# Optimization experiments

Hardware: AMD Instinct MI355X
Metric: run time of the kernel (lower is better)

The kernel has to match this reference:

```python
import jax, jax.numpy as jnp
import numpy as np

ALPHA = 0.2  # LeakyReLU negative slope
NEG_INF = jnp.float32(-9e15)


def setup_inputs() -> dict:
    key = jax.random.key(0)
    k1, k2, k3, k4, k5, k6 = jax.random.split(key, 6)
    B, N, F_in, F_out = 8, 2048, 256, 64
    h = jax.random.normal(k1, (B, N, F_in), dtype=jnp.float32)
    adj = jax.random.randint(k2, (B, N, N), 0, 2, dtype=jnp.int32)
    level = jax.random.uniform(k3, (B, N), dtype=jnp.float32)
    node_type = jax.random.uniform(k4, (B, N, N), dtype=jnp.float32)
    W = jax.random.normal(k5, (F_in, F_out), dtype=jnp.float32) * 1.414 / np.sqrt(F_in)
    a = jax.random.normal(k6, (2 * F_out, 1), dtype=jnp.float32) * 1.414 / np.sqrt(2 * F_out)
    return {"h": h, "adj": adj, "level": level, "node_type": node_type, "W": W, "a": a}


def reference(h, adj, level, node_type, W, a):
    # h: [B,N,Fin], adj/node_type: [B,N,N], level: [B,N], W: [Fin,Fout], a: [2*Fout,1]
    F_out = W.shape[1]
    Wh = jnp.einsum('bnf,fo->bno', h, W)  # [B,N,Fout]
    # Additive attention decomposed: e[b,i,j] = a1.Wh_i + a2.Wh_j (no O(N^2*2F) tensor)
    a1 = a[:F_out, 0]
    a2 = a[F_out:, 0]
    f1 = Wh @ a1  # [B,N]
    f2 = Wh @ a2  # [B,N]
    e = jax.nn.leaky_relu(f1[:, :, None] + f2[:, None, :], negative_slope=ALPHA)  # [B,N,N]
    # gat_our=True path: node_type scales scores, level scales Wh
    e = e * node_type
    Wh = Wh * level[:, :, None]
    attention = jnp.where(adj > 0, e, NEG_INF)
    attention = jax.nn.softmax(attention, axis=1)  # faithful: original softmax over dim=1
    # dropout p=0 / eval mode -> identity
    h_prime = jnp.einsum('bij,bjo->bio', attention, Wh)  # [B,N,Fout]
    return jax.nn.relu(h_prime)  # concat=True
```

## Files before the change

kernel.cpp:

```cpp
#include <hip/hip_runtime.h>

#define BB 8
#define NN 2048
#define FIN 256
#define FO 64

typedef short short8_t __attribute__((ext_vector_type(8)));
typedef float float4_t __attribute__((ext_vector_type(4)));

__device__ __forceinline__ unsigned short f2bf(float x) {
  unsigned int u = __float_as_uint(x);
  unsigned int r = (u + 0x7fffu + ((u >> 16) & 1u)) >> 16;
  return (unsigned short)r;
}

__global__ __launch_bounds__(256) void k1_gemm(
    const float* __restrict__ h,
    const float* __restrict__ level,
    const float* __restrict__ W,
    const float* __restrict__ a,
    float* __restrict__ V, float* __restrict__ f1, float* __restrict__ f2)
{
  __shared__ float hs[64 * 65];
  __shared__ float wsm[64 * 64];
  __shared__ float parts[2 * 1040];
  int t = threadIdx.x;
  int b = blockIdx.x >> 5;
  int i0 = (blockIdx.x & 31) * 64;
  int ti = t & 15, to = t >> 4;
  int srow = t >> 2;
  int sf0 = (t & 3) * 16;
  float acc[4][4] = {};

  for (int fc = 0; fc < FIN; fc += 64) {
    const float* hp = h + (size_t)(b * NN + i0 + srow) * FIN + fc + sf0;
    float4 h0 = *(const float4*)hp;
    float4 h1 = *(const float4*)(hp + 4);
    float4 h2 = *(const float4*)(hp + 8);
    float4 h3 = *(const float4*)(hp + 12);
    float* hd = &hs[srow * 65 + sf0];
    hd[0] = h0.x; hd[1] = h0.y; hd[2] = h0.z; hd[3] = h0.w;
    hd[4] = h1.x; hd[5] = h1.y; hd[6] = h1.z; hd[7] = h1.w;
    hd[8] = h2.x; hd[9] = h2.y; hd[10] = h2.z; hd[11] = h2.w;
    hd[12] = h3.x; hd[13] = h3.y; hd[14] = h3.z; hd[15] = h3.w;

    const float* wp = W + (size_t)(fc + srow) * FO + sf0;
    float4 w0 = *(const float4*)wp;
    float4 w1 = *(const float4*)(wp + 4);
    float4 w2 = *(const float4*)(wp + 8);
    float4 w3 = *(const float4*)(wp + 12);
    float* wd = &wsm[srow * 64 + sf0];
    *(float4*)(wd + 0) = w0; *(float4*)(wd + 4) = w1;
    *(float4*)(wd + 8) = w2; *(float4*)(wd + 12) = w3;
    __syncthreads();

    #pragma unroll 4
    for (int f = 0; f < 64; ++f) {
      float hv0 = hs[(ti * 4 + 0) * 65 + f];
      float hv1 = hs[(ti * 4 + 1) * 65 + f];
      float hv2 = hs[(ti * 4 + 2) * 65 + f];
      float hv3 = hs[(ti * 4 + 3) * 65 + f];
      float4 wv = *(const float4*)&wsm[f * 64 + to * 4];
      acc[0][0] += hv0 * wv.x; acc[0][1] += hv0 * wv.y; acc[0][2] += hv0 * wv.z; acc[0][3] += hv0 * wv.w;
      acc[1][0] += hv1 * wv.x; acc[1][1] += hv1 * wv.y; acc[1][2] += hv1 * wv.z; acc[1][3] += hv1 * wv.w;
      acc[2][0] += hv2 * wv.x; acc[2][1] += hv2 * wv.y; acc[2][2] += hv2 * wv.z; acc[2][3] += hv2 * wv.w;
      acc[3][0] += hv3 * wv.x; acc[3][1] += hv3 * wv.y; acc[3][2] += hv3 * wv.z; acc[3][3] += hv3 * wv.w;
    }
    __syncthreads();
  }

  float a1f0 = a[to * 4 + 0], a1f1 = a[to * 4 + 1];
  float a1f2 = a[to * 4 + 2], a1f3 = a[to * 4 + 3];
  float a2f0 = a[64 + to * 4 + 0], a2f1 = a[64 + to * 4 + 1];
  float a2f2 = a[64 + to * 4 + 2], a2f3 = a[64 + to * 4 + 3];
  #pragma unroll
  for (int r = 0; r < 4; ++r) {
    float p1 = acc[r][0] * a1f0 + acc[r][1] * a1f1 + acc[r][2] * a1f2 + acc[r][3] * a1f3;
    float p2 = acc[r][0] * a2f0 + acc[r][1] * a2f1 + acc[r][2] * a2f2 + acc[r][3] * a2f3;
    parts[to * 65 + ti * 4 + r] = p1;
    parts[1040 + to * 65 + ti * 4 + r] = p2;
  }
  __syncthreads();
  if (t < 64) {
    float s1 = 0.f, s2 = 0.f;
    #pragma unroll
    for (int g = 0; g < 16; ++g) { s1 += parts[g * 65 + t]; s2 += parts[1040 + g * 65 + t]; }
    f1[b * NN + i0 + t] = s1;
    f2[b * NN + i0 + t] = s2;
  }

  #pragma unroll
  for (int r = 0; r < 4; ++r) {
    float lv = level[b * NN + i0 + ti * 4 + r];
    float4 vv;
    vv.x = acc[r][0] * lv; vv.y = acc[r][1] * lv; vv.z = acc[r][2] * lv; vv.w = acc[r][3] * lv;
    *(float4*)&V[(size_t)(b * NN + i0 + ti * 4 + r) * FO + to * 4] = vv;
  }
}

template <int STORE_U>
__global__ __launch_bounds__(512) void k2_stats(
    const int* __restrict__ adj,
    const float* __restrict__ ntp,
    const float* __restrict__ f1,
    const float* __restrict__ f2,
    const float* __restrict__ V,
    unsigned short* __restrict__ vf,
    unsigned short* __restrict__ u_bf,
    unsigned char* __restrict__ bits)
{
  __shared__ float red[512 * 9];
  __shared__ float sinv[64];
  int t = threadIdx.x;
  int b = blockIdx.x >> 5;
  int jt = blockIdx.x & 31;
  int j0 = jt * 64;
  int tj = t & 7, isub = t >> 3;
  int j8 = j0 + tj * 8;

  float f2v[8];
  #pragma unroll
  for (int e = 0; e < 8; ++e) f2v[e] = f2[b * NN + j8 + e];
  float acc8[8] = {0, 0, 0, 0, 0, 0, 0, 0};

  for (int i = isub; i < NN; i += 64) {
    size_t base = (size_t)(b * NN + i);
    const int* ap = adj + base * NN + j8;
    int4 a0 = *(const int4*)ap;
    int4 a1 = *(const int4*)(ap + 4);
    const float* npp = ntp + base * NN + j8;
    float4 n0 = *(const float4*)npp;
    float4 n1 = *(const float4*)(npp + 4);
    float f1v = f1[base];
    float ntf[8] = {n0.x, n0.y, n0.z, n0.w, n1.x, n1.y, n1.z, n1.w};
    int am[8] = {a0.x, a0.y, a0.z, a0.w, a1.x, a1.y, a1.z, a1.w};
    float uv[8];
    unsigned int mb = 0;
    #pragma unroll
    for (int e = 0; e < 8; ++e) {
      float x = f1v + f2v[e];
      x = fmaxf(x, 0.2f * x);
      float E = x * ntf[e];
      bool m = am[e] > 0;
      float u = m ? __expf(E) : 0.0f;
      uv[e] = u;
      acc8[e] += u;
      mb |= (m ? 1u : 0u) << e;
    }
    if (STORE_U) {
      uint4 pk;
      pk.x = (unsigned int)f2bf(uv[0]) | ((unsigned int)f2bf(uv[1]) << 16);
      pk.y = (unsigned int)f2bf(uv[2]) | ((unsigned int)f2bf(uv[3]) << 16);
      pk.z = (unsigned int)f2bf(uv[4]) | ((unsigned int)f2bf(uv[5]) << 16);
      pk.w = (unsigned int)f2bf(uv[6]) | ((unsigned int)f2bf(uv[7]) << 16);
      *(uint4*)(u_bf + base * NN + j8) = pk;
    } else {
      bits[base * (NN / 8) + jt * 8 + tj] = (unsigned char)mb;
    }
  }

  #pragma unroll
  for (int e = 0; e < 8; ++e) red[t * 9 + e] = acc8[e];
  __syncthreads();
  if (t < 64) {
    int tjj = t >> 3, ee = t & 7;
    float s = 0.f;
    for (int is = 0; is < 64; ++is) s += red[(is * 8 + tjj) * 9 + ee];
    sinv[t] = (s > 0.f) ? (1.0f / s) : 0.0f;
  }
  __syncthreads();

  int kl = t >> 8;
  int ng = (t >> 6) & 3;
  int l = t & 63;
  int kk = jt * 2 + kl;
  int jb = kl * 32 + ((l >> 4) * 8);
  int o = ng * 16 + (l & 15);
  unsigned int pk[4];
  #pragma unroll
  for (int p = 0; p < 4; ++p) {
    int jr0 = jb + 2 * p, jr1 = jb + 2 * p + 1;
    float v0 = V[(size_t)(b * NN + j0 + jr0) * FO + o] * sinv[jr0];
    float v1 = V[(size_t)(b * NN + j0 + jr1) * FO + o] * sinv[jr1];
    pk[p] = (unsigned int)f2bf(v0) | ((unsigned int)f2bf(v1) << 16);
  }
  *(uint4*)(vf + (size_t)(((b * 64 + kk) * 4 + ng) * 64 + l) * 8) =
      make_uint4(pk[0], pk[1], pk[2], pk[3]);
}

__global__ __launch_bounds__(256) void k3_agg_u(
    const unsigned short* __restrict__ u_bf,
    const unsigned short* __restrict__ vf,
    float* __restrict__ outp)
{
  __shared__ float red[4 * 16 * 68];
  int t = threadIdx.x;
  int b = blockIdx.x >> 7;
  int i0 = (blockIdx.x & 127) * 16;
  int w = t >> 6, l = t & 63;
  int col = l & 15, quad = l >> 4;
  const unsigned short* urow = u_bf + (size_t)(b * NN + i0 + col) * NN + quad * 8;
  const unsigned short* vbase = vf + (size_t)(b * 64) * 2048 + l * 8;
  float4_t acc0 = {0, 0, 0, 0}, acc1 = {0, 0, 0, 0}, acc2 = {0, 0, 0, 0}, acc3 = {0, 0, 0, 0};

  for (int s = 0; s < 16; ++s) {
    int kk = w * 16 + s;
    short8_t A = *(const short8_t*)(urow + kk * 32);
    const unsigned short* vb = vbase + (size_t)kk * 2048;
    short8_t bf0 = *(const short8_t*)(vb);
    short8_t bf1 = *(const short8_t*)(vb + 512);
    short8_t bf2 = *(const short8_t*)(vb + 1024);
    short8_t bf3 = *(const short8_t*)(vb + 1536);
    acc0 = __builtin_amdgcn_mfma_f32_16x16x32_bf16(A, bf0, acc0, 0, 0, 0);
    acc1 = __builtin_amdgcn_mfma_f32_16x16x32_bf16(A, bf1, acc1, 0, 0, 0);
    acc2 = __builtin_amdgcn_mfma_f32_16x16x32_bf16(A, bf2, acc2, 0, 0, 0);
    acc3 = __builtin_amdgcn_mfma_f32_16x16x32_bf16(A, bf3, acc3, 0, 0, 0);
  }

  #pragma unroll
  for (int r = 0; r < 4; ++r) {
    int rowi = quad * 4 + r;
    red[w * 1088 + rowi * 68 + 0 + col] = acc0[r];
    red[w * 1088 + rowi * 68 + 16 + col] = acc1[r];
    red[w * 1088 + rowi * 68 + 32 + col] = acc2[r];
    red[w * 1088 + rowi * 68 + 48 + col] = acc3[r];
  }
  __syncthreads();

  int row = t >> 4, o4 = (t & 15) * 4;
  const float* rp = &red[row * 68 + o4];
  float4 s0 = *(const float4*)(rp);
  float4 s1 = *(const float4*)(rp + 1088);
  float4 s2 = *(const float4*)(rp + 2176);
  float4 s3 = *(const float4*)(rp + 3264);
  float4 o;
  o.x = fmaxf(s0.x + s1.x + s2.x + s3.x, 0.0f);
  o.y = fmaxf(s0.y + s1.y + s2.y + s3.y, 0.0f);
  o.z = fmaxf(s0.z + s1.z + s2.z + s3.z, 0.0f);
  o.w = fmaxf(s0.w + s1.w + s2.w + s3.w, 0.0f);
  *(float4*)&outp[(size_t)(b * NN + i0 + row) * FO + o4] = o;
}

__global__ __launch_bounds__(256) void k3_agg_b(
    const float* __restrict__ ntp,
    const unsigned char* __restrict__ bits,
    const float* __restrict__ f1,
    const float* __restrict__ f2,
    const unsigned short* __restrict__ vf,
    float* __restrict__ outp)
{
  __shared__ float red[4 * 16 * 68];
  int t = threadIdx.x;
  int b = blockIdx.x >> 7;
  int i0 = (blockIdx.x & 127) * 16;
  int w = t >> 6, l = t & 63;
  int col = l & 15, quad = l >> 4;
  int gi = b * NN + i0 + col;
  float f1v = f1[gi];
  const float* ntrow = ntp + (size_t)gi * NN;
  const unsigned char* brow = bits + (size_t)gi * (NN / 8);
  float4_t acc0 = {0, 0, 0, 0}, acc1 = {0, 0, 0, 0}, acc2 = {0, 0, 0, 0}, acc3 = {0, 0, 0, 0};

  for (int s = 0; s < 16; ++s) {
    int kk = w * 16 + s;
    int jq = kk * 32 + quad * 8;
    unsigned int m8 = brow[jq >> 3];
    float4 n0 = *(const float4*)(ntrow + jq);
    float4 n1 = *(const float4*)(ntrow + jq + 4);
    float4 g0 = *(const float4*)(f2 + b * NN + jq);
    float4 g1 = *(const float4*)(f2 + b * NN + jq + 4);
    float f2v[8] = {g0.x, g0.y, g0.z, g0.w, g1.x, g1.y, g1.z, g1.w};
    float ntf[8] = {n0.x, n0.y, n0.z, n0.w, n1.x, n1.y, n1.z, n1.w};
    union { unsigned int u[4]; short8_t v; } A;
    #pragma unroll
    for (int p = 0; p < 4; ++p) {
      int e0 = 2 * p, e1 = 2 * p + 1;
      float x0 = f1v + f2v[e0]; x0 = fmaxf(x0, 0.2f * x0);
      float u0 = ((m8 >> e0) & 1u) ? __expf(x0 * ntf[e0]) : 0.0f;
      float x1 = f1v + f2v[e1]; x1 = fmaxf(x1, 0.2f * x1);
      float u1 = ((m8 >> e1) & 1u) ? __expf(x1 * ntf[e1]) : 0.0f;
      A.u[p] = (unsigned int)f2bf(u0) | ((unsigned int)f2bf(u1) << 16);
    }
    const unsigned short* vb = vf + (size_t)(b * 64 + kk) * 2048 + l * 8;
    short8_t bf0 = *(const short8_t*)(vb);
    short8_t bf1 = *(const short8_t*)(vb + 512);
    short8_t bf2 = *(const short8_t*)(vb + 1024);
    short8_t bf3 = *(const short8_t*)(vb + 1536);
    acc0 = __builtin_amdgcn_mfma_f32_16x16x32_bf16(A.v, bf0, acc0, 0, 0, 0);
    acc1 = __builtin_amdgcn_mfma_f32_16x16x32_bf16(A.v, bf1, acc1, 0, 0, 0);
    acc2 = __builtin_amdgcn_mfma_f32_16x16x32_bf16(A.v, bf2, acc2, 0, 0, 0);
    acc3 = __builtin_amdgcn_mfma_f32_16x16x32_bf16(A.v, bf3, acc3, 0, 0, 0);
  }

  #pragma unroll
  for (int r = 0; r < 4; ++r) {
    int rowi = quad * 4 + r;
    red[w * 1088 + rowi * 68 + 0 + col] = acc0[r];
    red[w * 1088 + rowi * 68 + 16 + col] = acc1[r];
    red[w * 1088 + rowi * 68 + 32 + col] = acc2[r];
    red[w * 1088 + rowi * 68 + 48 + col] = acc3[r];
  }
  __syncthreads();

  int row = t >> 4, o4 = (t & 15) * 4;
  const float* rp = &red[row * 68 + o4];
  float4 s0 = *(const float4*)(rp);
  float4 s1 = *(const float4*)(rp + 1088);
  float4 s2 = *(const float4*)(rp + 2176);
  float4 s3 = *(const float4*)(rp + 3264);
  float4 o;
  o.x = fmaxf(s0.x + s1.x + s2.x + s3.x, 0.0f);
  o.y = fmaxf(s0.y + s1.y + s2.y + s3.y, 0.0f);
  o.z = fmaxf(s0.z + s1.z + s2.z + s3.z, 0.0f);
  o.w = fmaxf(s0.w + s1.w + s2.w + s3.w, 0.0f);
  *(float4*)&outp[(size_t)(b * NN + i0 + row) * FO + o4] = o;
}

extern "C" void kernel_launch(void* const* d_in, const int* in_sizes, int n_in,
                              void* d_out, int out_size, void* d_ws, size_t ws_size,
                              hipStream_t stream) {
  const float* h = (const float*)d_in[0];
  const int* adj = (const int*)d_in[1];
  const float* level = (const float*)d_in[2];
  const float* ntm = (const float*)d_in[3];
  const float* W = (const float*)d_in[4];
  const float* a = (const float*)d_in[5];
  float* outp = (float*)d_out;

  float* V = (float*)d_ws;
  float* f1 = V + (size_t)BB * NN * FO;
  float* f2 = f1 + BB * NN;
  unsigned short* vf = (unsigned short*)(f2 + BB * NN);
  char* tail = (char*)(vf + (size_t)BB * NN * FO);
  size_t fixed = (size_t)(tail - (char*)d_ws);
  size_t need_u = fixed + (size_t)BB * NN * NN * 2;
  bool big = (ws_size >= need_u);

  k1_gemm<<<256, 256, 0, stream>>>(h, level, W, a, V, f1, f2);
  if (big) {
    unsigned short* u_bf = (unsigned short*)tail;
    k2_stats<1><<<256, 512, 0, stream>>>(adj, ntm, f1, f2, V, vf, u_bf, nullptr);
    k3_agg_u<<<1024, 256, 0, stream>>>(u_bf, vf, outp);
  } else {
    unsigned char* bits = (unsigned char*)tail;
    k2_stats<0><<<256, 512, 0, stream>>>(adj, ntm, f1, f2, V, vf, nullptr, bits);
    k3_agg_b<<<1024, 256, 0, stream>>>(ntm, bits, f1, f2, vf, outp);
  }
}
```

Baseline: 351.7 us.

## Split column-stats pass over row chunks with atomics and separate V packing

The stats kernel now splits the 2048 rows into 8 chunks, giving 2048 blocks instead of 256, and accumulates column sums into a zeroed global buffer with atomicAdd. The V normalization and bf16 packing move into a new kernel that runs after all partial sums are complete. The projection GEMM is also retiled to 16 rows per block, reading W directly from global memory, which gives 1024 blocks. The aim is to fill the GPU's compute units on the bandwidth-heavy adjacency and node_type scan, at the cost of two extra launches and atomic traffic.

```diff
diff --git a/kernel.cpp b/kernel.cpp
--- a/kernel.cpp
+++ b/kernel.cpp
@@ -12,6 +12,10 @@
   unsigned int u = __float_as_uint(x);
   unsigned int r = (u + 0x7fffu + ((u >> 16) & 1u)) >> 16;
   return (unsigned short)r;
+}
+
+__global__ __launch_bounds__(256) void k0_zero(float* __restrict__ scol) {
+  scol[blockIdx.x * 256 + threadIdx.x] = 0.0f;
 }
 
 __global__ __launch_bounds__(256) void k1_gemm(
@@ -21,99 +25,77 @@
     const float* __restrict__ a,
     float* __restrict__ V, float* __restrict__ f1, float* __restrict__ f2)
 {
-  __shared__ float hs[64 * 65];
-  __shared__ float wsm[64 * 64];
-  __shared__ float parts[2 * 1040];
-  int t = threadIdx.x;
-  int b = blockIdx.x >> 5;
-  int i0 = (blockIdx.x & 31) * 64;
-  int ti = t & 15, to = t >> 4;
-  int srow = t >> 2;
-  int sf0 = (t & 3) * 16;
-  float acc[4][4] = {};
-
-  for (int fc = 0; fc < FIN; fc += 64) {
-    const float* hp = h + (size_t)(b * NN + i0 + srow) * FIN + fc + sf0;
-    float4 h0 = *(const float4*)hp;
-    float4 h1 = *(const float4*)(hp + 4);
-    float4 h2 = *(const float4*)(hp + 8);
-    float4 h3 = *(const float4*)(hp + 12);
-    float* hd = &hs[srow * 65 + sf0];
-    hd[0] = h0.x; hd[1] = h0.y; hd[2] = h0.z; hd[3] = h0.w;
-    hd[4] = h1.x; hd[5] = h1.y; hd[6] = h1.z; hd[7] = h1.w;
-    hd[8] = h2.x; hd[9] = h2.y; hd[10] = h2.z; hd[11] = h2.w;
-    hd[12] = h3.x; hd[13] = h3.y; hd[14] = h3.z; hd[15] = h3.w;
-
-    const float* wp = W + (size_t)(fc + srow) * FO + sf0;
-    float4 w0 = *(const float4*)wp;
-    float4 w1 = *(const float4*)(wp + 4);
-    float4 w2 = *(const float4*)(wp + 8);
-    float4 w3 = *(const float4*)(wp + 12);
-    float* wd = &wsm[srow * 64 + sf0];
-    *(float4*)(wd + 0) = w0; *(float4*)(wd + 4) = w1;
-    *(float4*)(wd + 8) = w2; *(float4*)(wd + 12) = w3;
-    __syncthreads();
-
-    #pragma unroll 4
-    for (int f = 0; f < 64; ++f) {
-      float hv0 = hs[(ti * 4 + 0) * 65 + f];
-      float hv1 = hs[(ti * 4 + 1) * 65 + f];
-      float hv2 = hs[(ti * 4 + 2) * 65 + f];
-      float hv3 = hs[(ti * 4 + 3) * 65 + f];
-      float4 wv = *(const float4*)&wsm[f * 64 + to * 4];
-      acc[0][0] += hv0 * wv.x; acc[0][1] += hv0 * wv.y; acc[0][2] += hv0 * wv.z; acc[0][3] += hv0 * wv.w;
-      acc[1][0] += hv1 * wv.x; acc[1][1] += hv1 * wv.y; acc[1][2] += hv1 * wv.z; acc[1][3] += hv1 * wv.w;
-      acc[2][0] += hv2 * wv.x; acc[2][1] += hv2 * wv.y; acc[2][2] += hv2 * wv.z; acc[2][3] += hv2 * wv.w;
-      acc[3][0] += hv3 * wv.x; acc[3][1] += hv3 * wv.y; acc[3][2] += hv3 * wv.z; acc[3][3] += hv3 * wv.w;
+  __shared__ float hs[16 * 260];
+  __shared__ float parts1[16 * 17];
+  __shared__ float parts2[16 * 17];
+  int t = threadIdx.x;
+  int b = blockIdx.x >> 7;
+  int i0 = (blockIdx.x & 127) * 16;
+
+  {
+    int r_ld = t >> 4, f0 = (t & 15) * 16;
+    const float* hp = h + (size_t)(b * NN + i0 + r_ld) * FIN + f0;
+    float4 x0 = *(const float4*)(hp);
+    float4 x1 = *(const float4*)(hp + 4);
+    float4 x2 = *(const float4*)(hp + 8);
+    float4 x3 = *(const float4*)(hp + 12);
+    float* hd = &hs[r_ld * 260 + f0];
+    *(float4*)(hd + 0) = x0; *(float4*)(hd + 4) = x1;
+    *(float4*)(hd + 8) = x2; *(float4*)(hd + 12) = x3;
+  }
+  __syncthreads();
+
+  int r = t >> 4;
+  int c4 = (t & 15) * 4;
+  float4 acc = {0, 0, 0, 0};
+
+  for (int f = 0; f < FIN; f += 8) {
+    float4 hv0 = *(const float4*)&hs[r * 260 + f];
+    float4 hv1 = *(const float4*)&hs[r * 260 + f + 4];
+    float hvv[8] = {hv0.x, hv0.y, hv0.z, hv0.w, hv1.x, hv1.y, hv1.z, hv1.w};
+    #pragma unroll
+    for (int k = 0; k < 8; ++k) {
+      float4 wv = *(const float4*)&W[(size_t)(f + k) * FO + c4];
+      acc.x += hvv[k] * wv.x; acc.y += hvv[k] * wv.y;
+      acc.z += hvv[k] * wv.z; acc.w += hvv[k] * wv.w;
     }
-    __syncthreads();
-  }
-
-  float a1f0 = a[to * 4 + 0], a1f1 = a[to * 4 + 1];
-  float a1f2 = a[to * 4 + 2], a1f3 = a[to * 4 + 3];
-  float a2f0 = a[64 + to * 4 + 0], a2f1 = a[64 + to * 4 + 1];
-  float a2f2 = a[64 + to * 4 + 2], a2f3 = a[64 + to * 4 + 3];
-  #pragma unroll
-  for (int r = 0; r < 4; ++r) {
-    float p1 = acc[r][0] * a1f0 + acc[r][1] * a1f1 + acc[r][2] * a1f2 + acc[r][3] * a1f3;
-    float p2 = acc[r][0] * a2f0 + acc[r][1] * a2f1 + acc[r][2] * a2f2 + acc[r][3] * a2f3;
-    parts[to * 65 + ti * 4 + r] = p1;
-    parts[1040 + to * 65 + ti * 4 + r] = p2;
-  }
-  __syncthreads();
-  if (t < 64) {
+  }
+
+  float p1 = acc.x * a[c4] + acc.y * a[c4 + 1] + acc.z * a[c4 + 2] + acc.w * a[c4 + 3];
+  float p2 = acc.x * a[64 + c4] + acc.y * a[64 + c4 + 1] +
+             acc.z * a[64 + c4 + 2] + acc.w * a[64 + c4 + 3];
+  parts1[r * 17 + (t & 15)] = p1;
+  parts2[r * 17 + (t & 15)] = p2;
+  __syncthreads();
+  if (t < 16) {
     float s1 = 0.f, s2 = 0.f;
     #pragma unroll
-    for (int g = 0; g < 16; ++g) { s1 += parts[g * 65 + t]; s2 += parts[1040 + g * 65 + t]; }
+    for (int g = 0; g < 16; ++g) { s1 += parts1[t * 17 + g]; s2 += parts2[t * 17 + g]; }
     f1[b * NN + i0 + t] = s1;
     f2[b * NN + i0 + t] = s2;
   }
 
-  #pragma unroll
-  for (int r = 0; r < 4; ++r) {
-    float lv = level[b * NN + i0 + ti * 4 + r];
-    float4 vv;
-    vv.x = acc[r][0] * lv; vv.y = acc[r][1] * lv; vv.z = acc[r][2] * lv; vv.w = acc[r][3] * lv;
-    *(float4*)&V[(size_t)(b * NN + i0 + ti * 4 + r) * FO + to * 4] = vv;
-  }
+  float lv = level[b * NN + i0 + r];
+  float4 vv = {acc.x * lv, acc.y * lv, acc.z * lv, acc.w * lv};
+  *(float4*)&V[(size_t)(b * NN + i0 + r) * FO + c4] = vv;
 }
 
 template <int STORE_U>
-__global__ __launch_bounds__(512) void k2_stats(
+__global__ __launch_bounds__(512) void k2a_stats(
     const int* __restrict__ adj,
     const float* __restrict__ ntp,
     const float* __restrict__ f1,
     const float* __restrict__ f2,
-    const float* __restrict__ V,
-    unsigned short* __restrict__ vf,
     unsigned short* __restrict__ u_bf,
-    unsigned char* __restrict__ bits)
+    unsigned char* __restrict__ bits,
+    float* __restrict__ scol)
 {
   __shared__ float red[512 * 9];
-  __shared__ float sinv[64];
-  int t = threadIdx.x;
-  int b = blockIdx.x >> 5;
-  int jt = blockIdx.x & 31;
+  int t = threadIdx.x;
+  int blk = blockIdx.x;
+  int chunk = blk >> 8;
+  int b = (blk >> 5) & 7;
+  int jt = blk & 31;
   int j0 = jt * 64;
   int tj = t & 7, isub = t >> 3;
   int j8 = j0 + tj * 8;
@@ -123,7 +105,9 @@
   for (int e = 0; e < 8; ++e) f2v[e] = f2[b * NN + j8 + e];
   float acc8[8] = {0, 0, 0, 0, 0, 0, 0, 0};
 
-  for (int i = isub; i < NN; i += 64) {
+  #pragma unroll
+  for (int ii = 0; ii < 4; ++ii) {
+    int i = chunk * 256 + ii * 64 + isub;
     size_t base = (size_t)(b * NN + i);
     const int* ap = adj + base * NN + j8;
     int4 a0 = *(const int4*)ap;
@@ -166,22 +150,32 @@
     int tjj = t >> 3, ee = t & 7;
     float s = 0.f;
     for (int is = 0; is < 64; ++is) s += red[(is * 8 + tjj) * 9 + ee];
-    sinv[t] = (s > 0.f) ? (1.0f / s) : 0.0f;
-  }
-  __syncthreads();
-
-  int kl = t >> 8;
-  int ng = (t >> 6) & 3;
+    atomicAdd(&scol[b * NN + j0 + t], s);
+  }
+}
+
+__global__ __launch_bounds__(256) void k2b_pack(
+    const float* __restrict__ V,
+    const float* __restrict__ scol,
+    unsigned short* __restrict__ vf)
+{
+  int t = threadIdx.x;
+  int b = blockIdx.x >> 6;
+  int kk = blockIdx.x & 63;
+  int ng = t >> 6;
   int l = t & 63;
-  int kk = jt * 2 + kl;
-  int jb = kl * 32 + ((l >> 4) * 8);
+  int jb = kk * 32 + ((l >> 4) * 8);
   int o = ng * 16 + (l & 15);
   unsigned int pk[4];
   #pragma unroll
   for (int p = 0; p < 4; ++p) {
     int jr0 = jb + 2 * p, jr1 = jb + 2 * p + 1;
-    float v0 = V[(size_t)(b * NN + j0 + jr0) * FO + o] * sinv[jr0];
-    float v1 = V[(size_t)(b * NN + j0 + jr1) * FO + o] * sinv[jr1];
+    float s0 = scol[b * NN + jr0];
+    float s1 = scol[b * NN + jr1];
+    float i0 = (s0 > 0.f) ? (1.0f / s0) : 0.0f;
+    float i1 = (s1 > 0.f) ? (1.0f / s1) : 0.0f;
+    float v0 = V[(size_t)(b * NN + jr0) * FO + o] * i0;
+    float v1 = V[(size_t)(b * NN + jr1) * FO + o] * i1;
     pk[p] = (unsigned int)f2bf(v0) | ((unsigned int)f2bf(v1) << 16);
   }
   *(uint4*)(vf + (size_t)(((b * 64 + kk) * 4 + ng) * 64 + l) * 8) =
@@ -330,20 +324,24 @@
   float* V = (float*)d_ws;
   float* f1 = V + (size_t)BB * NN * FO;
   float* f2 = f1 + BB * NN;
-  unsigned short* vf = (unsigned short*)(f2 + BB * NN);
+  float* scol = f2 + BB * NN;
+  unsigned short* vf = (unsigned short*)(scol + BB * NN);
   char* tail = (char*)(vf + (size_t)BB * NN * FO);
   size_t fixed = (size_t)(tail - (char*)d_ws);
   size_t need_u = fixed + (size_t)BB * NN * NN * 2;
   bool big = (ws_size >= need_u);
 
-  k1_gemm<<<256, 256, 0, stream>>>(h, level, W, a, V, f1, f2);
+  k0_zero<<<64, 256, 0, stream>>>(scol);
+  k1_gemm<<<1024, 256, 0, stream>>>(h, level, W, a, V, f1, f2);
   if (big) {
     unsigned short* u_bf = (unsigned short*)tail;
-    k2_stats<1><<<256, 512, 0, stream>>>(adj, ntm, f1, f2, V, vf, u_bf, nullptr);
+    k2a_stats<1><<<2048, 512, 0, stream>>>(adj, ntm, f1, f2, u_bf, nullptr, scol);
+    k2b_pack<<<512, 256, 0, stream>>>(V, scol, vf);
     k3_agg_u<<<1024, 256, 0, stream>>>(u_bf, vf, outp);
   } else {
     unsigned char* bits = (unsigned char*)tail;
-    k2_stats<0><<<256, 512, 0, stream>>>(adj, ntm, f1, f2, V, vf, nullptr, bits);
+    k2a_stats<0><<<2048, 512, 0, stream>>>(adj, ntm, f1, f2, nullptr, bits, scol);
+    k2b_pack<<<512, 256, 0, stream>>>(V, scol, vf);
     k3_agg_b<<<1024, 256, 0, stream>>>(ntm, bits, f1, f2, vf, outp);
   }
 }
```

After: 371.4 us. 1.06x slower.
